# Optimization experiments

Hardware: AMD Instinct MI355X
Metric: run time of the kernel (lower is better)

The kernel has to match this reference:

```python
import jax, jax.numpy as jnp
import numpy as np

# SLAYER neuron / simulation constants (from netParams yaml)
THETA = 10.0      # spike threshold
TAU_SR = 10.0     # PSP (SRM) time constant, ms
TS = 1.0          # simulation time step, ms
TAU_RHO = 1.0     # surrogate-gradient width
SCALE_RHO = 1.0   # surrogate-gradient scale
N_TIME_BINS = 300 # tSample / Ts


@jax.custom_vjp
def spike_fn(u):
    # Hard threshold forward; surrogate gradient backward (SLAYER escape-rate pdf).
    return (u >= THETA).astype(u.dtype)

def _spike_fwd(u):
    return spike_fn(u), u

def _spike_bwd(u, g):
    return (g * SCALE_RHO * jnp.exp(-jnp.abs(u - THETA) / TAU_RHO),)

spike_fn.defvjp(_spike_fwd, _spike_bwd)


def psp(x):
    # Causal leaky-integrator (first-order SRM) filter over time.
    # x: [B, T, F] -> u[t] = decay * u[t-1] + x[t]
    decay = jnp.exp(jnp.asarray(-TS / TAU_SR, x.dtype))
    xT = jnp.swapaxes(x, 0, 1)  # [T, B, F]
    def step(u, xt):
        u = decay * u + xt
        return u, u
    _, out = jax.lax.scan(step, jnp.zeros_like(xT[0]), xT)
    return jnp.swapaxes(out, 0, 1)  # [B, T, F]


def rate_encode(inp, n_time_bins, key):
    # Bernoulli rate coding: spike prob per time bin = pixel intensity in [0,1].
    # inp: [B, C, H, W] -> spikes: [B, T, C*H*W]
    B = inp.shape[0]
    probs = inp.reshape(B, 1, -1)  # [B, 1, F]
    u = jax.random.uniform(key, (B, n_time_bins, probs.shape[-1]), dtype=inp.dtype)
    return (u < probs).astype(inp.dtype)


def setup_inputs() -> dict:
    key = jax.random.key(0)
    k1, k2, k3 = jax.random.split(key, 3)
    B, C, H, W = 32, 3, 32, 32
    F_in, F_hid, F_out = C * H * W, 410, 10
    inp = jax.random.uniform(k1, (B, C, H, W), dtype=jnp.float32)
    W1 = jax.random.normal(k2, (F_hid, F_in), dtype=jnp.float32) / np.sqrt(F_in).astype(np.float32)
    W2 = jax.random.normal(k3, (F_out, F_hid), dtype=jnp.float32) / np.sqrt(F_hid).astype(np.float32)
    return {"inp": inp, "W1": W1, "W2": W2}


def reference(inp, W1, W2):
    spikes = rate_encode(inp, N_TIME_BINS, jax.random.key(42))   # [B, T, 3072]
    a1 = jnp.einsum('btf,of->bto', spikes, W1)                    # dense per time bin
    s1 = spike_fn(psp(a1))                                        # [B, T, 410]
    a2 = jnp.einsum('btf,of->bto', s1, W2)
    s2 = spike_fn(psp(a2))                                        # [B, T, 10]
    return jnp.swapaxes(s2, 1, 2)                                 # [B, 10, T]
```

## Files before the change

### kernel.cpp

```cpp
#include <hip/hip_runtime.h>
#include <stdint.h>

#define B_SZ 32
#define T_SZ 300
#define F_IN 3072
#define F_HID 410
#define F_OUT 10
#define M_SZ (B_SZ * T_SZ)
#define N_PAD 448
#define KW (F_IN / 32)
#define TOTAL_ELEMS (B_SZ * T_SZ * F_IN)
#define N_WORDS (TOTAL_ELEMS / 32)
#define A2_STRIDE 16
#define NCHUNK 10
#define CLEN 30
#define NKB (F_IN / 256)
#define MT_CNT (M_SZ / 64)
#define W1_BLOCKS 672
#define RNG_BLOCKS 14400

#define DECAY 0.90483741803595957f
#define THETA 10.0f
#define KS2 (0x1BD11BDAu ^ 42u)

typedef __attribute__((ext_vector_type(8))) int i32x8;
typedef __attribute__((ext_vector_type(16))) float f32x16;

#define TF_R(r) { x0 += x1; \
  asm("v_alignbit_b32 %0, %1, %1, %2" : "=v"(x1) : "v"(x1), "n"(32 - (r))); \
  x1 ^= x0; }

__device__ __forceinline__ uint32_t tf_bits(uint32_t x1i) {
  uint32_t x0 = 0u, x1 = x1i;
  TF_R(13) TF_R(15) TF_R(26) TF_R(6)
  x0 += 42u; x1 += KS2 + 1u;
  TF_R(17) TF_R(29) TF_R(16) TF_R(24)
  x0 += KS2; x1 += 2u;
  TF_R(13) TF_R(15) TF_R(26) TF_R(6)
  x1 += 42u + 3u;
  TF_R(17) TF_R(29) TF_R(16) TF_R(24)
  x0 += 42u; x1 += KS2 + 4u;
  TF_R(13) TF_R(15) TF_R(26) TF_R(6)
  x0 += KS2; x1 += 5u;
  return x0 ^ x1;
}

__device__ __forceinline__ void gld16(const void* g, void* l) {
  __builtin_amdgcn_global_load_lds(
      (const __attribute__((address_space(1))) uint32_t*)g,
      (__attribute__((address_space(3))) uint32_t*)l, 16, 0, 0);
}

__global__ __launch_bounds__(256) void prep(const float* __restrict__ inp,
                                            const float* __restrict__ W1,
                                            uint8_t* __restrict__ W1s,
                                            uint32_t* __restrict__ sbitsT) {
  if (blockIdx.x < W1_BLOCKS) {
    int idx = blockIdx.x * 256 + threadIdx.x;
    int g = idx * 8;
    int n = g / F_IN;
    int k = g - n * F_IN;
    uint32_t d0 = 0u, d1 = 0u;
    if (n < F_HID) {
      const float* s = W1 + (size_t)n * F_IN + k;
      float4 v0 = ((const float4*)s)[0];
      float4 v1 = ((const float4*)s)[1];
      int t0 = __builtin_amdgcn_cvt_pk_fp8_f32(v0.x, v0.y, 0, false);
      t0 = __builtin_amdgcn_cvt_pk_fp8_f32(v0.z, v0.w, t0, true);
      int t1 = __builtin_amdgcn_cvt_pk_fp8_f32(v1.x, v1.y, 0, false);
      t1 = __builtin_amdgcn_cvt_pk_fp8_f32(v1.z, v1.w, t1, true);
      d0 = (uint32_t)t0; d1 = (uint32_t)t1;
    }
    int nt = n >> 6, r = n & 63;
    int kb = k >> 8, c = (k >> 4) & 15, half = (k >> 3) & 1;
    size_t dst = ((((size_t)nt * NKB + kb) * 64 + r) * 16 + (c ^ (r & 15))) * 16 + half * 8;
    *(uint2*)(W1s + dst) = make_uint2(d0, d1);
  } else {
    uint32_t idx = (blockIdx.x - W1_BLOCKS) * 256u + threadIdx.x;
    uint32_t q = idx & 3u;
    uint32_t j = idx >> 2;
    uint32_t r = j & 63u;
    uint32_t t1 = j >> 6;
    uint32_t wi = t1 & 7u;
    uint32_t t2 = t1 >> 3;
    uint32_t kb = t2 % (uint32_t)NKB;
    uint32_t mt = t2 / (uint32_t)NKB;
    uint32_t m = mt * 64u + r;
    uint32_t b = m / (uint32_t)T_SZ;
    uint32_t f = (kb * 8u + wi) * 32u + q * 8u;
    const float* p = inp + b * F_IN + f;
    float4 va = ((const float4*)p)[0];
    float4 vb = ((const float4*)p)[1];
    uint32_t T0 = (uint32_t)ceilf(va.x * 8388608.0f);
    uint32_t T1 = (uint32_t)ceilf(va.y * 8388608.0f);
    uint32_t T2 = (uint32_t)ceilf(va.z * 8388608.0f);
    uint32_t T3 = (uint32_t)ceilf(va.w * 8388608.0f);
    uint32_t T4 = (uint32_t)ceilf(vb.x * 8388608.0f);
    uint32_t T5 = (uint32_t)ceilf(vb.y * 8388608.0f);
    uint32_t T6 = (uint32_t)ceilf(vb.z * 8388608.0f);
    uint32_t T7 = (uint32_t)ceilf(vb.w * 8388608.0f);
    uint32_t b42 = m * (uint32_t)F_IN + f + 42u;
    uint32_t w = 0u;
#define GEN(jj, Tn) { uint32_t bits = tf_bits(b42 + (jj)); \
  w |= ((bits >> 9) < (Tn)) ? (1u << (jj)) : 0u; }
    GEN(0, T0) GEN(1, T1) GEN(2, T2) GEN(3, T3)
    GEN(4, T4) GEN(5, T5) GEN(6, T6) GEN(7, T7)
#undef GEN
    ((uint8_t*)sbitsT)[idx] = (uint8_t)w;
  }
}

__global__ __launch_bounds__(256) void gemm1(const uint32_t* __restrict__ sbitsT,
                                             const uint8_t* __restrict__ W1s,
                                             float* __restrict__ a1) {
  __shared__ uint32_t sAT[8 * 64];
  __shared__ uint8_t sB[64 * 256];

  const int tid = threadIdx.x;
  const int mtile = blockIdx.x;
  const int nt = blockIdx.y;
  const int m0 = mtile * 64;
  const int n0 = nt * 64;
  const int wv = tid >> 6, lane = tid & 63;
  const int wm = (wv & 1) * 32, wn = (wv >> 1) * 32;
  const int l31 = lane & 31, lh = lane >> 5;

  const uint8_t* gB0 = W1s + (size_t)nt * NKB * 16384;
  const uint8_t* gA0 = (const uint8_t*)sbitsT + (size_t)mtile * NKB * 2048;

  f32x16 acc;
#pragma unroll
  for (int e = 0; e < 16; ++e) acc[e] = 0.0f;

  for (int kb = 0; kb < NKB; ++kb) {
    const uint8_t* gB = gB0 + (size_t)kb * 16384;
#pragma unroll
    for (int q = 0; q < 4; ++q)
      gld16(gB + (wv * 4 + q) * 1024 + lane * 16, &sB[(wv * 4 + q) * 1024]);
    if (wv < 2)
      gld16(gA0 + (size_t)kb * 2048 + wv * 1024 + lane * 16,
            (uint8_t*)sAT + wv * 1024);
    __syncthreads();
#pragma unroll
    for (int sub = 0; sub < 4; ++sub) {
      int row = wn + l31;
      int cb = sub * 4 + lh * 2;
      uint4 u0 = *(uint4*)&sB[row * 256 + (((cb + 0) ^ (row & 15)) << 4)];
      uint4 u1 = *(uint4*)&sB[row * 256 + (((cb + 1) ^ (row & 15)) << 4)];
      i32x8 bfr;
      bfr[0] = u0.x; bfr[1] = u0.y; bfr[2] = u0.z; bfr[3] = u0.w;
      bfr[4] = u1.x; bfr[5] = u1.y; bfr[6] = u1.z; bfr[7] = u1.w;
      uint32_t w = sAT[(sub * 2 + lh) * 64 + wm + l31];
      i32x8 afr;
#pragma unroll
      for (int j = 0; j < 8; ++j) {
        uint32_t n = (w >> (4 * j)) & 15u;
        afr[j] = (int)(((n * 0x204081u) & 0x01010101u) * 0x38u);
      }
      acc = __builtin_amdgcn_mfma_scale_f32_32x32x64_f8f6f4(
          afr, bfr, acc, 0, 0, 0, 127, 0, 127);
    }
    __syncthreads();
  }
  int col = n0 + wn + l31;
#pragma unroll
  for (int rg = 0; rg < 16; ++rg) {
    int row = m0 + wm + (rg & 3) + 8 * (rg >> 2) + 4 * lh;
    a1[(size_t)row * N_PAD + col] = acc[rg];
  }
}

__global__ __launch_bounds__(256) void psp1_partial(float* __restrict__ a1,
                                                    float* __restrict__ fin) {
  int idx = blockIdx.x * 256 + threadIdx.x;
  if (idx >= B_SZ * NCHUNK * N_PAD) return;
  int o = idx % N_PAD;
  int bc = idx / N_PAD;
  int c = bc % NCHUNK;
  int b = bc / NCHUNK;
  float* p = a1 + ((size_t)(b * T_SZ + c * CLEN)) * N_PAD + o;
  float u = 0.0f;
#pragma unroll
  for (int i = 0; i < CLEN; ++i) {
    u = __fadd_rn(__fmul_rn(DECAY, u), p[(size_t)i * N_PAD]);
    p[(size_t)i * N_PAD] = u;
  }
  fin[(size_t)bc * N_PAD + o] = u;
}

__global__ __launch_bounds__(256) void apply_gemm2(const float* __restrict__ a1,
                                                   const float* __restrict__ fin,
                                                   const float* __restrict__ W2,
                                                   float* __restrict__ a2) {
  __shared__ float sW2[F_OUT * F_HID];
  for (int i = threadIdx.x; i < F_OUT * F_HID; i += 256) sW2[i] = W2[i];
  __syncthreads();
  int m = blockIdx.x * 4 + (threadIdx.x >> 6);
  int lane = threadIdx.x & 63;
  int b = m / T_SZ, t = m % T_SZ;
  int c = t / CLEN, tl = t % CLEN;
  float d30 = 1.0f;
#pragma unroll
  for (int i = 0; i < CLEN; ++i) d30 *= DECAY;
  float dp = DECAY;
  for (int i = 0; i < tl; ++i) dp *= DECAY;
  float p[F_OUT];
#pragma unroll
  for (int o = 0; o < F_OUT; ++o) p[o] = 0.0f;
#pragma unroll
  for (int j = 0; j < 7; ++j) {
    int hh = lane + j * 64;
    float u = a1[(size_t)m * N_PAD + hh];
    if (c > 0) {
      float F = 0.0f;
      const float* f = fin + (size_t)b * NCHUNK * N_PAD + hh;
      for (int cc = 0; cc < c; ++cc)
        F = f[(size_t)cc * N_PAD] + d30 * F;
      u = __fadd_rn(u, __fmul_rn(dp, F));
    }
    bool valid = hh < F_HID;
    float s = (u >= THETA && valid) ? 1.0f : 0.0f;
    int hcl = valid ? hh : 0;
#pragma unroll
    for (int o = 0; o < F_OUT; ++o) p[o] = fmaf(s, sW2[o * F_HID + hcl], p[o]);
  }
#pragma unroll
  for (int o = 0; o < F_OUT; ++o)
#pragma unroll
    for (int s = 1; s < 64; s <<= 1) p[o] += __shfl_xor(p[o], s, 64);
  if (lane < F_OUT) a2[(size_t)m * A2_STRIDE + lane] = p[lane];
}

__global__ __launch_bounds__(128) void psp2(const float* __restrict__ a2,
                                            float* __restrict__ out) {
  __shared__ float chf[NCHUNK][F_OUT];
  __shared__ float seed[NCHUNK][F_OUT];
  int b = blockIdx.x;
  int tid = threadIdx.x;
  int o = tid / NCHUNK, c = tid % NCHUNK;
  const float* p = a2 + ((size_t)(b * T_SZ + c * CLEN)) * A2_STRIDE + o;
  float v[CLEN];
  float pa[CLEN];
  if (tid < F_OUT * NCHUNK) {
#pragma unroll
    for (int i = 0; i < CLEN; ++i) v[i] = p[(size_t)i * A2_STRIDE];
    float u = 0.0f;
#pragma unroll
    for (int i = 0; i < CLEN; ++i) {
      u = __fadd_rn(__fmul_rn(DECAY, u), v[i]);
      pa[i] = u;
    }
    chf[c][o] = u;
  }
  __syncthreads();
  if (tid < F_OUT) {
    float d30 = 1.0f;
#pragma unroll
    for (int i = 0; i < CLEN; ++i) d30 *= DECAY;
    float F = 0.0f;
    for (int cc = 0; cc < NCHUNK; ++cc) {
      F = chf[cc][tid] + d30 * F;
      seed[cc][tid] = F;
    }
  }
  __syncthreads();
  if (tid < F_OUT * NCHUNK) {
    float F = (c == 0) ? 0.0f : seed[c - 1][o];
    float dp = DECAY;
    float* q = out + (size_t)b * F_OUT * T_SZ + (size_t)o * T_SZ + c * CLEN;
#pragma unroll
    for (int i = 0; i < CLEN; ++i) {
      float u = (c == 0) ? pa[i] : __fadd_rn(pa[i], __fmul_rn(dp, F));
      q[i] = (u >= THETA) ? 1.0f : 0.0f;
      dp *= DECAY;
    }
  }
}

extern "C" void kernel_launch(void* const* d_in, const int* in_sizes, int n_in,
                              void* d_out, int out_size, void* d_ws, size_t ws_size,
                              hipStream_t stream) {
  const float* inp = (const float*)d_in[0];
  const float* W1  = (const float*)d_in[1];
  const float* W2  = (const float*)d_in[2];
  float* out = (float*)d_out;
  char* ws = (char*)d_ws;
  uint8_t* W1s = (uint8_t*)(ws);
  uint32_t* sbitsT = (uint32_t*)(ws + 1376256);
  float* a1 = (float*)(ws + 1376256 + 3686400);
  float* fin = a1 + (size_t)M_SZ * N_PAD;
  float* a2 = fin + (size_t)B_SZ * NCHUNK * N_PAD;

  prep<<<dim3(W1_BLOCKS + RNG_BLOCKS), dim3(256), 0, stream>>>(inp, W1, W1s, sbitsT);
  gemm1<<<dim3(MT_CNT, N_PAD / 64), dim3(256), 0, stream>>>(sbitsT, W1s, a1);
  psp1_partial<<<dim3((B_SZ * NCHUNK * N_PAD) / 256), dim3(256), 0, stream>>>(a1, fin);
  apply_gemm2<<<dim3(M_SZ / 4), dim3(256), 0, stream>>>(a1, fin, W2, a2);
  psp2<<<dim3(B_SZ), dim3(128), 0, stream>>>(a2, out);
}
```

Before: 173.6 us.

## Double-buffer gemm1 LDS tiles and read W2 directly in apply_gemm2

gemm1 now keeps two LDS buffers for the spike-bit and W1 tiles. It prefetches the next K block while the MFMAs run on the current one, which overlaps global loads with compute and drops one barrier per iteration. apply_gemm2 no longer copies all of W2 into shared memory in every block. It reads W2 straight from global memory and relies on the cache, removing a per-block staging cost and a barrier. The trade-offs are doubled LDS use in gemm1, which may lower occupancy, and a reliance on async loads finishing before the barrier.

Result: no change. 175.1 us (+0.9%).

```diff
diff --git a/kernel.cpp b/kernel.cpp
--- a/kernel.cpp
+++ b/kernel.cpp
@@ -113,8 +113,8 @@
 __global__ __launch_bounds__(256) void gemm1(const uint32_t* __restrict__ sbitsT,
                                              const uint8_t* __restrict__ W1s,
                                              float* __restrict__ a1) {
-  __shared__ uint32_t sAT[8 * 64];
-  __shared__ uint8_t sB[64 * 256];
+  __shared__ uint32_t sAT[2][8 * 64];
+  __shared__ uint8_t sB[2][64 * 256];
 
   const int tid = threadIdx.x;
   const int mtile = blockIdx.x;
@@ -132,25 +132,35 @@
 #pragma unroll
   for (int e = 0; e < 16; ++e) acc[e] = 0.0f;
 
+#pragma unroll
+  for (int q = 0; q < 4; ++q)
+    gld16(gB0 + (wv * 4 + q) * 1024 + lane * 16, &sB[0][(wv * 4 + q) * 1024]);
+  if (wv < 2)
+    gld16(gA0 + wv * 1024 + lane * 16, (uint8_t*)sAT[0] + wv * 1024);
+
   for (int kb = 0; kb < NKB; ++kb) {
-    const uint8_t* gB = gB0 + (size_t)kb * 16384;
-#pragma unroll
-    for (int q = 0; q < 4; ++q)
-      gld16(gB + (wv * 4 + q) * 1024 + lane * 16, &sB[(wv * 4 + q) * 1024]);
-    if (wv < 2)
-      gld16(gA0 + (size_t)kb * 2048 + wv * 1024 + lane * 16,
-            (uint8_t*)sAT + wv * 1024);
     __syncthreads();
+    if (kb + 1 < NKB) {
+      const int nb = (kb + 1) & 1;
+      const uint8_t* gB = gB0 + (size_t)(kb + 1) * 16384;
+#pragma unroll
+      for (int q = 0; q < 4; ++q)
+        gld16(gB + (wv * 4 + q) * 1024 + lane * 16, &sB[nb][(wv * 4 + q) * 1024]);
+      if (wv < 2)
+        gld16(gA0 + (size_t)(kb + 1) * 2048 + wv * 1024 + lane * 16,
+              (uint8_t*)sAT[nb] + wv * 1024);
+    }
+    const int bf = kb & 1;
 #pragma unroll
     for (int sub = 0; sub < 4; ++sub) {
       int row = wn + l31;
       int cb = sub * 4 + lh * 2;
-      uint4 u0 = *(uint4*)&sB[row * 256 + (((cb + 0) ^ (row & 15)) << 4)];
-      uint4 u1 = *(uint4*)&sB[row * 256 + (((cb + 1) ^ (row & 15)) << 4)];
+      uint4 u0 = *(uint4*)&sB[bf][row * 256 + (((cb + 0) ^ (row & 15)) << 4)];
+      uint4 u1 = *(uint4*)&sB[bf][row * 256 + (((cb + 1) ^ (row & 15)) << 4)];
       i32x8 bfr;
       bfr[0] = u0.x; bfr[1] = u0.y; bfr[2] = u0.z; bfr[3] = u0.w;
       bfr[4] = u1.x; bfr[5] = u1.y; bfr[6] = u1.z; bfr[7] = u1.w;
-      uint32_t w = sAT[(sub * 2 + lh) * 64 + wm + l31];
+      uint32_t w = sAT[bf][(sub * 2 + lh) * 64 + wm + l31];
       i32x8 afr;
 #pragma unroll
       for (int j = 0; j < 8; ++j) {
@@ -160,7 +170,6 @@
       acc = __builtin_amdgcn_mfma_scale_f32_32x32x64_f8f6f4(
           afr, bfr, acc, 0, 0, 0, 127, 0, 127);
     }
-    __syncthreads();
   }
   int col = n0 + wn + l31;
 #pragma unroll
@@ -192,9 +201,6 @@
                                                    const float* __restrict__ fin,
                                                    const float* __restrict__ W2,
                                                    float* __restrict__ a2) {
-  __shared__ float sW2[F_OUT * F_HID];
-  for (int i = threadIdx.x; i < F_OUT * F_HID; i += 256) sW2[i] = W2[i];
-  __syncthreads();
   int m = blockIdx.x * 4 + (threadIdx.x >> 6);
   int lane = threadIdx.x & 63;
   int b = m / T_SZ, t = m % T_SZ;
@@ -222,7 +228,7 @@
     float s = (u >= THETA && valid) ? 1.0f : 0.0f;
     int hcl = valid ? hh : 0;
 #pragma unroll
-    for (int o = 0; o < F_OUT; ++o) p[o] = fmaf(s, sW2[o * F_HID + hcl], p[o]);
+    for (int o = 0; o < F_OUT; ++o) p[o] = fmaf(s, W2[o * F_HID + hcl], p[o]);
   }
 #pragma unroll
   for (int o = 0; o < F_OUT; ++o)
```

## Replace chunked PSP1 with sequential scan emitting spike bitmasks; split prep kernels

Applied to the files above, without the earlier changes.

The chunked two-pass layer-1 PSP (partial scan plus carry fix-up inside the gemm2 kernel) is replaced by a single full-length scan per (batch, neuron). It ballots threshold crossings into packed bitmasks. gemm2 then reads those bits instead of re-reading a1 and recomputing carries, and reads W2 from global memory rather than staging it in shared memory. The combined prep kernel is also split into a W1 conversion launch and two RNG launches. The sequential 300-step scan exposes far less parallelism (only 56 blocks), which may cost latency, and the extra launches add overhead.

Measured after the change: 240.1 us. +38.3%, slower.

```diff
diff --git a/kernel.cpp b/kernel.cpp
--- a/kernel.cpp
+++ b/kernel.cpp
@@ -17,7 +17,8 @@
 #define NKB (F_IN / 256)
 #define MT_CNT (M_SZ / 64)
 #define W1_BLOCKS 672
-#define RNG_BLOCKS 14400
+#define RNG_THREADS (N_WORDS * 4)
+#define RNG_HALF (RNG_THREADS / 2)
 
 #define DECAY 0.90483741803595957f
 #define THETA 10.0f
@@ -51,63 +52,63 @@
       (__attribute__((address_space(3))) uint32_t*)l, 16, 0, 0);
 }
 
-__global__ __launch_bounds__(256) void prep(const float* __restrict__ inp,
-                                            const float* __restrict__ W1,
-                                            uint8_t* __restrict__ W1s,
-                                            uint32_t* __restrict__ sbitsT) {
-  if (blockIdx.x < W1_BLOCKS) {
-    int idx = blockIdx.x * 256 + threadIdx.x;
-    int g = idx * 8;
-    int n = g / F_IN;
-    int k = g - n * F_IN;
-    uint32_t d0 = 0u, d1 = 0u;
-    if (n < F_HID) {
-      const float* s = W1 + (size_t)n * F_IN + k;
-      float4 v0 = ((const float4*)s)[0];
-      float4 v1 = ((const float4*)s)[1];
-      int t0 = __builtin_amdgcn_cvt_pk_fp8_f32(v0.x, v0.y, 0, false);
-      t0 = __builtin_amdgcn_cvt_pk_fp8_f32(v0.z, v0.w, t0, true);
-      int t1 = __builtin_amdgcn_cvt_pk_fp8_f32(v1.x, v1.y, 0, false);
-      t1 = __builtin_amdgcn_cvt_pk_fp8_f32(v1.z, v1.w, t1, true);
-      d0 = (uint32_t)t0; d1 = (uint32_t)t1;
-    }
-    int nt = n >> 6, r = n & 63;
-    int kb = k >> 8, c = (k >> 4) & 15, half = (k >> 3) & 1;
-    size_t dst = ((((size_t)nt * NKB + kb) * 64 + r) * 16 + (c ^ (r & 15))) * 16 + half * 8;
-    *(uint2*)(W1s + dst) = make_uint2(d0, d1);
-  } else {
-    uint32_t idx = (blockIdx.x - W1_BLOCKS) * 256u + threadIdx.x;
-    uint32_t q = idx & 3u;
-    uint32_t j = idx >> 2;
-    uint32_t r = j & 63u;
-    uint32_t t1 = j >> 6;
-    uint32_t wi = t1 & 7u;
-    uint32_t t2 = t1 >> 3;
-    uint32_t kb = t2 % (uint32_t)NKB;
-    uint32_t mt = t2 / (uint32_t)NKB;
-    uint32_t m = mt * 64u + r;
-    uint32_t b = m / (uint32_t)T_SZ;
-    uint32_t f = (kb * 8u + wi) * 32u + q * 8u;
-    const float* p = inp + b * F_IN + f;
-    float4 va = ((const float4*)p)[0];
-    float4 vb = ((const float4*)p)[1];
-    uint32_t T0 = (uint32_t)ceilf(va.x * 8388608.0f);
-    uint32_t T1 = (uint32_t)ceilf(va.y * 8388608.0f);
-    uint32_t T2 = (uint32_t)ceilf(va.z * 8388608.0f);
-    uint32_t T3 = (uint32_t)ceilf(va.w * 8388608.0f);
-    uint32_t T4 = (uint32_t)ceilf(vb.x * 8388608.0f);
-    uint32_t T5 = (uint32_t)ceilf(vb.y * 8388608.0f);
-    uint32_t T6 = (uint32_t)ceilf(vb.z * 8388608.0f);
-    uint32_t T7 = (uint32_t)ceilf(vb.w * 8388608.0f);
-    uint32_t b42 = m * (uint32_t)F_IN + f + 42u;
-    uint32_t w = 0u;
+__global__ __launch_bounds__(256) void prep_w1(const float* __restrict__ W1,
+                                               uint8_t* __restrict__ W1s) {
+  int idx = blockIdx.x * 256 + threadIdx.x;
+  int g = idx * 8;
+  int n = g / F_IN;
+  int k = g - n * F_IN;
+  uint32_t d0 = 0u, d1 = 0u;
+  if (n < F_HID) {
+    const float* s = W1 + (size_t)n * F_IN + k;
+    float4 v0 = ((const float4*)s)[0];
+    float4 v1 = ((const float4*)s)[1];
+    int t0 = __builtin_amdgcn_cvt_pk_fp8_f32(v0.x, v0.y, 0, false);
+    t0 = __builtin_amdgcn_cvt_pk_fp8_f32(v0.z, v0.w, t0, true);
+    int t1 = __builtin_amdgcn_cvt_pk_fp8_f32(v1.x, v1.y, 0, false);
+    t1 = __builtin_amdgcn_cvt_pk_fp8_f32(v1.z, v1.w, t1, true);
+    d0 = (uint32_t)t0; d1 = (uint32_t)t1;
+  }
+  int nt = n >> 6, r = n & 63;
+  int kb = k >> 8, c = (k >> 4) & 15, half = (k >> 3) & 1;
+  size_t dst = ((((size_t)nt * NKB + kb) * 64 + r) * 16 + (c ^ (r & 15))) * 16 + half * 8;
+  *(uint2*)(W1s + dst) = make_uint2(d0, d1);
+}
+
+__global__ __launch_bounds__(256) void rng(const float* __restrict__ inp,
+                                           uint32_t* __restrict__ sbitsT,
+                                           uint32_t off) {
+  uint32_t idx = off + blockIdx.x * 256u + threadIdx.x;
+  uint32_t q = idx & 3u;
+  uint32_t j = idx >> 2;
+  uint32_t r = j & 63u;
+  uint32_t t1 = j >> 6;
+  uint32_t wi = t1 & 7u;
+  uint32_t t2 = t1 >> 3;
+  uint32_t kb = t2 % (uint32_t)NKB;
+  uint32_t mt = t2 / (uint32_t)NKB;
+  uint32_t m = mt * 64u + r;
+  uint32_t b = m / (uint32_t)T_SZ;
+  uint32_t f = (kb * 8u + wi) * 32u + q * 8u;
+  const float* p = inp + b * F_IN + f;
+  float4 va = ((const float4*)p)[0];
+  float4 vb = ((const float4*)p)[1];
+  uint32_t T0 = (uint32_t)ceilf(va.x * 8388608.0f);
+  uint32_t T1 = (uint32_t)ceilf(va.y * 8388608.0f);
+  uint32_t T2 = (uint32_t)ceilf(va.z * 8388608.0f);
+  uint32_t T3 = (uint32_t)ceilf(va.w * 8388608.0f);
+  uint32_t T4 = (uint32_t)ceilf(vb.x * 8388608.0f);
+  uint32_t T5 = (uint32_t)ceilf(vb.y * 8388608.0f);
+  uint32_t T6 = (uint32_t)ceilf(vb.z * 8388608.0f);
+  uint32_t T7 = (uint32_t)ceilf(vb.w * 8388608.0f);
+  uint32_t b42 = m * (uint32_t)F_IN + f + 42u;
+  uint32_t w = 0u;
 #define GEN(jj, Tn) { uint32_t bits = tf_bits(b42 + (jj)); \
   w |= ((bits >> 9) < (Tn)) ? (1u << (jj)) : 0u; }
-    GEN(0, T0) GEN(1, T1) GEN(2, T2) GEN(3, T3)
-    GEN(4, T4) GEN(5, T5) GEN(6, T6) GEN(7, T7)
+  GEN(0, T0) GEN(1, T1) GEN(2, T2) GEN(3, T3)
+  GEN(4, T4) GEN(5, T5) GEN(6, T6) GEN(7, T7)
 #undef GEN
-    ((uint8_t*)sbitsT)[idx] = (uint8_t)w;
-  }
+  ((uint8_t*)sbitsT)[idx] = (uint8_t)w;
 }
 
 __global__ __launch_bounds__(256) void gemm1(const uint32_t* __restrict__ sbitsT,
@@ -170,59 +171,42 @@
   }
 }
 
-__global__ __launch_bounds__(256) void psp1_partial(float* __restrict__ a1,
-                                                    float* __restrict__ fin) {
-  int idx = blockIdx.x * 256 + threadIdx.x;
-  if (idx >= B_SZ * NCHUNK * N_PAD) return;
-  int o = idx % N_PAD;
-  int bc = idx / N_PAD;
-  int c = bc % NCHUNK;
-  int b = bc / NCHUNK;
-  float* p = a1 + ((size_t)(b * T_SZ + c * CLEN)) * N_PAD + o;
+__global__ __launch_bounds__(256) void psp_spike1(const float* __restrict__ a1,
+                                                  uint32_t* __restrict__ s1b) {
+  int g = blockIdx.x * 256 + threadIdx.x;
+  int b = g / N_PAD;
+  int o = g - b * N_PAD;
+  int lane = threadIdx.x & 63;
+  int j = o >> 6;
+  const float* p = a1 + (size_t)b * T_SZ * N_PAD + o;
+  uint32_t* q = s1b + ((size_t)b * T_SZ) * 16 + j * 2;
   float u = 0.0f;
-#pragma unroll
-  for (int i = 0; i < CLEN; ++i) {
-    u = __fadd_rn(__fmul_rn(DECAY, u), p[(size_t)i * N_PAD]);
-    p[(size_t)i * N_PAD] = u;
-  }
-  fin[(size_t)bc * N_PAD + o] = u;
-}
-
-__global__ __launch_bounds__(256) void apply_gemm2(const float* __restrict__ a1,
-                                                   const float* __restrict__ fin,
-                                                   const float* __restrict__ W2,
-                                                   float* __restrict__ a2) {
-  __shared__ float sW2[F_OUT * F_HID];
-  for (int i = threadIdx.x; i < F_OUT * F_HID; i += 256) sW2[i] = W2[i];
-  __syncthreads();
+#pragma unroll 4
+  for (int t = 0; t < T_SZ; ++t) {
+    u = __fadd_rn(__fmul_rn(DECAY, u), p[(size_t)t * N_PAD]);
+    unsigned long long mask = __ballot(u >= THETA);
+    if (lane == 0) *(uint2*)q = make_uint2((uint32_t)mask, (uint32_t)(mask >> 32));
+    q += 16;
+  }
+}
+
+__global__ __launch_bounds__(256) void gemm2(const uint32_t* __restrict__ s1b,
+                                             const float* __restrict__ W2,
+                                             float* __restrict__ a2) {
   int m = blockIdx.x * 4 + (threadIdx.x >> 6);
   int lane = threadIdx.x & 63;
-  int b = m / T_SZ, t = m % T_SZ;
-  int c = t / CLEN, tl = t % CLEN;
-  float d30 = 1.0f;
-#pragma unroll
-  for (int i = 0; i < CLEN; ++i) d30 *= DECAY;
-  float dp = DECAY;
-  for (int i = 0; i < tl; ++i) dp *= DECAY;
+  const uint32_t* row = s1b + (size_t)m * 16;
   float p[F_OUT];
 #pragma unroll
   for (int o = 0; o < F_OUT; ++o) p[o] = 0.0f;
 #pragma unroll
   for (int j = 0; j < 7; ++j) {
+    uint32_t wbits = row[j * 2 + (lane >> 5)];
+    float s = (float)((wbits >> (lane & 31)) & 1u);
     int hh = lane + j * 64;
-    float u = a1[(size_t)m * N_PAD + hh];
-    if (c > 0) {
-      float F = 0.0f;
-      const float* f = fin + (size_t)b * NCHUNK * N_PAD + hh;
-      for (int cc = 0; cc < c; ++cc)
-        F = f[(size_t)cc * N_PAD] + d30 * F;
-      u = __fadd_rn(u, __fmul_rn(dp, F));
-    }
-    bool valid = hh < F_HID;
-    float s = (u >= THETA && valid) ? 1.0f : 0.0f;
-    int hcl = valid ? hh : 0;
-#pragma unroll
-    for (int o = 0; o < F_OUT; ++o) p[o] = fmaf(s, sW2[o * F_HID + hcl], p[o]);
+    int hcl = (hh < F_HID) ? hh : 0;
+#pragma unroll
+    for (int o = 0; o < F_OUT; ++o) p[o] = fmaf(s, W2[o * F_HID + hcl], p[o]);
   }
 #pragma unroll
   for (int o = 0; o < F_OUT; ++o)
@@ -288,12 +272,14 @@
   uint8_t* W1s = (uint8_t*)(ws);
   uint32_t* sbitsT = (uint32_t*)(ws + 1376256);
   float* a1 = (float*)(ws + 1376256 + 3686400);
-  float* fin = a1 + (size_t)M_SZ * N_PAD;
-  float* a2 = fin + (size_t)B_SZ * NCHUNK * N_PAD;
-
-  prep<<<dim3(W1_BLOCKS + RNG_BLOCKS), dim3(256), 0, stream>>>(inp, W1, W1s, sbitsT);
+  uint32_t* s1b = (uint32_t*)(ws + 1376256 + 3686400 + 17203200);
+  float* a2 = (float*)(ws + 1376256 + 3686400 + 17203200 + 614400);
+
+  prep_w1<<<dim3(W1_BLOCKS), dim3(256), 0, stream>>>(W1, W1s);
+  rng<<<dim3(RNG_HALF / 256), dim3(256), 0, stream>>>(inp, sbitsT, 0u);
+  rng<<<dim3(RNG_HALF / 256), dim3(256), 0, stream>>>(inp, sbitsT, (uint32_t)RNG_HALF);
   gemm1<<<dim3(MT_CNT, N_PAD / 64), dim3(256), 0, stream>>>(sbitsT, W1s, a1);
-  psp1_partial<<<dim3((B_SZ * NCHUNK * N_PAD) / 256), dim3(256), 0, stream>>>(a1, fin);
-  apply_gemm2<<<dim3(M_SZ / 4), dim3(256), 0, stream>>>(a1, fin, W2, a2);
+  psp_spike1<<<dim3((B_SZ * N_PAD) / 256), dim3(256), 0, stream>>>(a1, s1b);
+  gemm2<<<dim3(M_SZ / 4), dim3(256), 0, stream>>>(s1b, W2, a2);
   psp2<<<dim3(B_SZ), dim3(128), 0, stream>>>(a2, out);
 }
```

## Fuse chunked PSP scan into GEMM1 epilogue and store potentials as bf16

Applied to the files above, without the earlier changes.

GEMM1 now uses 60-row M tiles aligned to 30-step chunks. Its epilogue stages the accumulator tile in shared memory and runs the per-chunk leaky-integrator scan there, writing chunk finals directly. This removes the separate psp1_partial kernel and its read-modify-write pass over a1. The partial potentials are stored as bf16 to halve traffic into apply_gemm2, and the spike bits are relaid so each lane loads its A word straight from global memory instead of staging it in LDS. The risks are that bf16 rounding near the threshold can flip spikes, and the 60-row tile wastes 4 of the MFMA's 64 rows.

New measurement: 185.1 us. +6.7%, slower.

```diff
diff --git a/kernel.cpp b/kernel.cpp
--- a/kernel.cpp
+++ b/kernel.cpp
@@ -7,15 +7,13 @@
 #define F_HID 410
 #define F_OUT 10
 #define M_SZ (B_SZ * T_SZ)
+#define M_PAD 9664
 #define N_PAD 448
-#define KW (F_IN / 32)
-#define TOTAL_ELEMS (B_SZ * T_SZ * F_IN)
-#define N_WORDS (TOTAL_ELEMS / 32)
 #define A2_STRIDE 16
 #define NCHUNK 10
 #define CLEN 30
 #define NKB (F_IN / 256)
-#define MT_CNT (M_SZ / 64)
+#define MT_CNT (M_SZ / 60)
 #define W1_BLOCKS 672
 #define RNG_BLOCKS 14400
 
@@ -54,7 +52,7 @@
 __global__ __launch_bounds__(256) void prep(const float* __restrict__ inp,
                                             const float* __restrict__ W1,
                                             uint8_t* __restrict__ W1s,
-                                            uint32_t* __restrict__ sbitsT) {
+                                            uint32_t* __restrict__ sbits) {
   if (blockIdx.x < W1_BLOCKS) {
     int idx = blockIdx.x * 256 + threadIdx.x;
     int g = idx * 8;
@@ -78,16 +76,15 @@
   } else {
     uint32_t idx = (blockIdx.x - W1_BLOCKS) * 256u + threadIdx.x;
     uint32_t q = idx & 3u;
-    uint32_t j = idx >> 2;
-    uint32_t r = j & 63u;
-    uint32_t t1 = j >> 6;
-    uint32_t wi = t1 & 7u;
-    uint32_t t2 = t1 >> 3;
-    uint32_t kb = t2 % (uint32_t)NKB;
-    uint32_t mt = t2 / (uint32_t)NKB;
-    uint32_t m = mt * 64u + r;
+    uint32_t t = idx >> 2;
+    uint32_t pos = t & 7u;
+    uint32_t t2 = t >> 3;
+    uint32_t kb = t2 / (uint32_t)M_SZ;
+    uint32_t m = t2 - kb * (uint32_t)M_SZ;
+    uint32_t sub = pos & 3u, lh = pos >> 2;
+    uint32_t wi = sub * 2u + lh;
+    uint32_t f = kb * 256u + wi * 32u + q * 8u;
     uint32_t b = m / (uint32_t)T_SZ;
-    uint32_t f = (kb * 8u + wi) * 32u + q * 8u;
     const float* p = inp + b * F_IN + f;
     float4 va = ((const float4*)p)[0];
     float4 vb = ((const float4*)p)[1];
@@ -106,27 +103,30 @@
     GEN(0, T0) GEN(1, T1) GEN(2, T2) GEN(3, T3)
     GEN(4, T4) GEN(5, T5) GEN(6, T6) GEN(7, T7)
 #undef GEN
-    ((uint8_t*)sbitsT)[idx] = (uint8_t)w;
-  }
-}
-
-__global__ __launch_bounds__(256) void gemm1(const uint32_t* __restrict__ sbitsT,
+    ((uint8_t*)sbits)[(((size_t)kb * M_PAD + m) * 8 + pos) * 4 + q] = (uint8_t)w;
+  }
+}
+
+__global__ __launch_bounds__(256) void gemm1(const uint32_t* __restrict__ sbits,
                                              const uint8_t* __restrict__ W1s,
-                                             float* __restrict__ a1) {
-  __shared__ uint32_t sAT[8 * 64];
-  __shared__ uint8_t sB[64 * 256];
+                                             uint16_t* __restrict__ ap1,
+                                             float* __restrict__ fin) {
+  __shared__ union {
+    uint8_t B[64 * 256];
+    float red[64 * 68];
+  } sm;
 
   const int tid = threadIdx.x;
   const int mtile = blockIdx.x;
   const int nt = blockIdx.y;
-  const int m0 = mtile * 64;
+  const int m0 = mtile * 60;
   const int n0 = nt * 64;
   const int wv = tid >> 6, lane = tid & 63;
   const int wm = (wv & 1) * 32, wn = (wv >> 1) * 32;
   const int l31 = lane & 31, lh = lane >> 5;
 
   const uint8_t* gB0 = W1s + (size_t)nt * NKB * 16384;
-  const uint8_t* gA0 = (const uint8_t*)sbitsT + (size_t)mtile * NKB * 2048;
+  const uint32_t* gA = sbits + ((size_t)(m0 + wm + l31)) * 8 + lh * 4;
 
   f32x16 acc;
 #pragma unroll
@@ -136,21 +136,20 @@
     const uint8_t* gB = gB0 + (size_t)kb * 16384;
 #pragma unroll
     for (int q = 0; q < 4; ++q)
-      gld16(gB + (wv * 4 + q) * 1024 + lane * 16, &sB[(wv * 4 + q) * 1024]);
-    if (wv < 2)
-      gld16(gA0 + (size_t)kb * 2048 + wv * 1024 + lane * 16,
-            (uint8_t*)sAT + wv * 1024);
+      gld16(gB + (wv * 4 + q) * 1024 + lane * 16, &sm.B[(wv * 4 + q) * 1024]);
+    uint4 aw = *(const uint4*)(gA + (size_t)kb * M_PAD * 8);
     __syncthreads();
+    const uint32_t awv[4] = {aw.x, aw.y, aw.z, aw.w};
 #pragma unroll
     for (int sub = 0; sub < 4; ++sub) {
       int row = wn + l31;
       int cb = sub * 4 + lh * 2;
-      uint4 u0 = *(uint4*)&sB[row * 256 + (((cb + 0) ^ (row & 15)) << 4)];
-      uint4 u1 = *(uint4*)&sB[row * 256 + (((cb + 1) ^ (row & 15)) << 4)];
+      uint4 u0 = *(uint4*)&sm.B[row * 256 + (((cb + 0) ^ (row & 15)) << 4)];
+      uint4 u1 = *(uint4*)&sm.B[row * 256 + (((cb + 1) ^ (row & 15)) << 4)];
       i32x8 bfr;
       bfr[0] = u0.x; bfr[1] = u0.y; bfr[2] = u0.z; bfr[3] = u0.w;
       bfr[4] = u1.x; bfr[5] = u1.y; bfr[6] = u1.z; bfr[7] = u1.w;
-      uint32_t w = sAT[(sub * 2 + lh) * 64 + wm + l31];
+      uint32_t w = awv[sub];
       i32x8 afr;
 #pragma unroll
       for (int j = 0; j < 8; ++j) {
@@ -162,39 +161,35 @@
     }
     __syncthreads();
   }
-  int col = n0 + wn + l31;
-#pragma unroll
-  for (int rg = 0; rg < 16; ++rg) {
-    int row = m0 + wm + (rg & 3) + 8 * (rg >> 2) + 4 * lh;
-    a1[(size_t)row * N_PAD + col] = acc[rg];
-  }
-}
-
-__global__ __launch_bounds__(256) void psp1_partial(float* __restrict__ a1,
-                                                    float* __restrict__ fin) {
-  int idx = blockIdx.x * 256 + threadIdx.x;
-  if (idx >= B_SZ * NCHUNK * N_PAD) return;
-  int o = idx % N_PAD;
-  int bc = idx / N_PAD;
-  int c = bc % NCHUNK;
-  int b = bc / NCHUNK;
-  float* p = a1 + ((size_t)(b * T_SZ + c * CLEN)) * N_PAD + o;
-  float u = 0.0f;
-#pragma unroll
-  for (int i = 0; i < CLEN; ++i) {
-    u = __fadd_rn(__fmul_rn(DECAY, u), p[(size_t)i * N_PAD]);
-    p[(size_t)i * N_PAD] = u;
-  }
-  fin[(size_t)bc * N_PAD + o] = u;
-}
-
-__global__ __launch_bounds__(256) void apply_gemm2(const float* __restrict__ a1,
+  {
+    int col = wn + l31;
+#pragma unroll
+    for (int rg = 0; rg < 16; ++rg) {
+      int row = wm + (rg & 3) + 8 * (rg >> 2) + 4 * lh;
+      sm.red[row * 68 + col] = acc[rg];
+    }
+  }
+  __syncthreads();
+  if (tid < 128) {
+    int ch = tid >> 6, c = tid & 63;
+    int b = m0 / T_SZ;
+    int cg = (m0 % T_SZ) / CLEN + ch;
+    uint16_t* dst = ap1 + (size_t)(m0 + ch * CLEN) * N_PAD + n0 + c;
+    float u = 0.0f;
+#pragma unroll
+    for (int i = 0; i < CLEN; ++i) {
+      u = __fadd_rn(__fmul_rn(DECAY, u), sm.red[(ch * CLEN + i) * 68 + c]);
+      uint32_t ub = __float_as_uint(u);
+      dst[(size_t)i * N_PAD] = (uint16_t)((ub + 0x7FFFu + ((ub >> 16) & 1u)) >> 16);
+    }
+    fin[((size_t)b * NCHUNK + cg) * N_PAD + n0 + c] = u;
+  }
+}
+
+__global__ __launch_bounds__(256) void apply_gemm2(const uint16_t* __restrict__ ap1,
                                                    const float* __restrict__ fin,
                                                    const float* __restrict__ W2,
                                                    float* __restrict__ a2) {
-  __shared__ float sW2[F_OUT * F_HID];
-  for (int i = threadIdx.x; i < F_OUT * F_HID; i += 256) sW2[i] = W2[i];
-  __syncthreads();
   int m = blockIdx.x * 4 + (threadIdx.x >> 6);
   int lane = threadIdx.x & 63;
   int b = m / T_SZ, t = m % T_SZ;
@@ -210,7 +205,7 @@
 #pragma unroll
   for (int j = 0; j < 7; ++j) {
     int hh = lane + j * 64;
-    float u = a1[(size_t)m * N_PAD + hh];
+    float u = __uint_as_float(((uint32_t)ap1[(size_t)m * N_PAD + hh]) << 16);
     if (c > 0) {
       float F = 0.0f;
       const float* f = fin + (size_t)b * NCHUNK * N_PAD + hh;
@@ -222,7 +217,7 @@
     float s = (u >= THETA && valid) ? 1.0f : 0.0f;
     int hcl = valid ? hh : 0;
 #pragma unroll
-    for (int o = 0; o < F_OUT; ++o) p[o] = fmaf(s, sW2[o * F_HID + hcl], p[o]);
+    for (int o = 0; o < F_OUT; ++o) p[o] = fmaf(s, W2[o * F_HID + hcl], p[o]);
   }
 #pragma unroll
   for (int o = 0; o < F_OUT; ++o)
@@ -286,14 +281,13 @@
   float* out = (float*)d_out;
   char* ws = (char*)d_ws;
   uint8_t* W1s = (uint8_t*)(ws);
-  uint32_t* sbitsT = (uint32_t*)(ws + 1376256);
-  float* a1 = (float*)(ws + 1376256 + 3686400);
-  float* fin = a1 + (size_t)M_SZ * N_PAD;
-  float* a2 = fin + (size_t)B_SZ * NCHUNK * N_PAD;
-
-  prep<<<dim3(W1_BLOCKS + RNG_BLOCKS), dim3(256), 0, stream>>>(inp, W1, W1s, sbitsT);
-  gemm1<<<dim3(MT_CNT, N_PAD / 64), dim3(256), 0, stream>>>(sbitsT, W1s, a1);
-  psp1_partial<<<dim3((B_SZ * NCHUNK * N_PAD) / 256), dim3(256), 0, stream>>>(a1, fin);
-  apply_gemm2<<<dim3(M_SZ / 4), dim3(256), 0, stream>>>(a1, fin, W2, a2);
+  uint32_t* sbits = (uint32_t*)(ws + 1376256);
+  uint16_t* ap1 = (uint16_t*)(ws + 1376256 + 3710976);
+  float* fin = (float*)(ws + 1376256 + 3710976 + 8601600);
+  float* a2 = (float*)(ws + 1376256 + 3710976 + 8601600 + 573440);
+
+  prep<<<dim3(W1_BLOCKS + RNG_BLOCKS), dim3(256), 0, stream>>>(inp, W1, W1s, sbits);
+  gemm1<<<dim3(MT_CNT, N_PAD / 64), dim3(256), 0, stream>>>(sbits, W1s, ap1, fin);
+  apply_gemm2<<<dim3(M_SZ / 4), dim3(256), 0, stream>>>(ap1, fin, W2, a2);
   psp2<<<dim3(B_SZ), dim3(128), 0, stream>>>(a2, out);
 }
```
